# Kernel tuning notes

Measured on AMD Instinct MI355X. Metric: run time of the kernel, lower is better.

## Reference

```python
import jax, jax.numpy as jnp
import numpy as np

IN_CH = 512; OUT_CH = 512; NOISE_SIZE = 512; K = 3; A = 0.2
B = 4; H = 32
_G = float(np.sqrt(2.0 / (1.0 + A * A)))                 # leaky_relu gain, a=0.2
CONV_SCALE = _G / float(np.sqrt(IN_CH * K * K))          # equal-lr kaiming scale (fan_in = in_ch*3*3)
MS_SCALE = float(np.sqrt(2.0 / (NOISE_SIZE + IN_CH)))    # equal-lr xavier scale on make_s linear
RGB_SCALE = _G * float(np.sqrt(2.0 / (OUT_CH + 3)))      # equal-lr xavier scale on 1x1 to_rgb


def upsample2x(x):
    # torch F.interpolate(scale_factor=2, mode='bilinear', align_corners=False)
    b, c, h, w = x.shape
    return jax.image.resize(x, (b, c, 2 * h, 2 * w), method='bilinear')


def mod_conv(x, style, weight, bias, ms_w, ms_b, w_scale, demodulate, pad):
    # style -> per-sample input-channel scales s: (B, Cin)
    s = style @ (ms_w.T * MS_SCALE) + ms_b
    Wmod = (weight * w_scale)[None] * s[:, None, :, None, None]   # (B, Cout, Cin, k, k)
    if demodulate:
        d = jax.lax.rsqrt(jnp.sum(Wmod * Wmod, axis=(2, 3, 4)) + 1e-8)
        Wmod = Wmod * d[:, :, None, None, None]
    conv1 = lambda xi, wi: jax.lax.conv_general_dilated(
        xi[None], wi, (1, 1), [(pad, pad), (pad, pad)],
        dimension_numbers=('NCHW', 'OIHW', 'NCHW'))[0]
    y = jax.vmap(conv1)(x, Wmod)                                   # per-sample weights == grouped conv
    return y + bias[None, :, None, None]


def lrelu(x):
    return jnp.where(x >= 0, x, A * x)


def setup_inputs() -> dict:
    key = jax.random.key(0)
    ks = jax.random.split(key, 19)
    r = lambda i, shape: jax.random.normal(ks[i], shape, dtype=jnp.float32)
    return {
        'maps': r(0, (B, IN_CH, H, H)),
        'w': r(1, (B, NOISE_SIZE)),
        'rgb': r(2, (B, 3, H, H)),
        'noise0': r(3, (B, 1, 2 * H, 2 * H)),
        'noise1': r(4, (B, 1, 2 * H, 2 * H)),
        'conv0_w': r(5, (OUT_CH, IN_CH, K, K)),
        'conv0_b': 0.1 * r(6, (OUT_CH,)),
        'ms0_w': r(7, (IN_CH, NOISE_SIZE)),
        'ms0_b': jnp.ones((IN_CH,), jnp.float32),
        'ns0': 0.1 * r(8, (OUT_CH,)),
        'conv1_w': r(9, (OUT_CH, OUT_CH, K, K)),
        'conv1_b': 0.1 * r(10, (OUT_CH,)),
        'ms1_w': r(11, (OUT_CH, NOISE_SIZE)),
        'ms1_b': jnp.ones((OUT_CH,), jnp.float32),
        'ns1': 0.1 * r(12, (OUT_CH,)),
        'rgb_w': r(13, (3, OUT_CH, 1, 1)),
        'rgb_b': 0.1 * r(14, (3,)),
        'msr_w': r(15, (OUT_CH, NOISE_SIZE)),
        'msr_b': jnp.ones((OUT_CH,), jnp.float32),
    }


def reference(maps, w, rgb, noise0, noise1,
              conv0_w, conv0_b, ms0_w, ms0_b, ns0,
              conv1_w, conv1_b, ms1_w, ms1_b, ns1,
              rgb_w, rgb_b, msr_w, msr_b):
    # upsample branch (upsample=True)
    rgb = upsample2x(rgb)
    maps = upsample2x(maps)
    # layer 0: modulated conv -> noise -> leaky relu
    h = mod_conv(maps, w, conv0_w, conv0_b, ms0_w, ms0_b, CONV_SCALE, True, 1)
    h = lrelu(h + ns0[None, :, None, None] * noise0)
    # layer 1
    h = mod_conv(h, w, conv1_w, conv1_b, ms1_w, ms1_b, CONV_SCALE, True, 1)
    h = lrelu(h + ns1[None, :, None, None] * noise1)
    # to_rgb: 1x1 modulated conv, no demodulation
    rgb_out = rgb + mod_conv(h, w, rgb_w, rgb_b, msr_w, msr_b, RGB_SCALE, False, 0)
    return (rgb_out, h)
```

## Files before the change

### kernel.cpp

```cpp
#include <hip/hip_runtime.h>
#include <stdint.h>


#define BATCH 4
#define CH 512
#define NPP 4356
#define HOUT_OFF 49152

static constexpr double G_GAIN = 1.3867504905630728;
static constexpr float CONV_SCALE_F = (float)(G_GAIN / 67.88225099390857);
static constexpr float MS_SCALE_F = 0.044194173824159216f;
static constexpr float RGB_SCALE_F = (float)(G_GAIN * 1.4142135623730951 / 22.693611435820433);

typedef __attribute__((ext_vector_type(8))) short short8;
typedef __attribute__((ext_vector_type(4))) float floatx4;
typedef __attribute__((ext_vector_type(16))) float floatx16;

#define OFF_S0     256
#define OFF_S1     (OFF_S0 + 8192)
#define OFF_SR     (OFF_S1 + 8192)
#define OFF_D0     (OFF_SR + 8192)
#define OFF_D1     (OFF_D0 + 8192)
#define OFF_B0F    (OFF_D1 + 8192)
#define OFF_B1F    (OFF_B0F + 2048)
#define OFF_NS0F   (OFF_B1F + 2048)
#define OFF_NS1F   (OFF_NS0F + 2048)
#define OFF_WMODR  (OFF_NS1F + 2048)
#define OFF_N0F    (OFF_WMODR + 24576)
#define OFF_N1F    (OFF_N0F + 65536)
#define OFF_WT0    (OFF_N1F + 65536)
#define WT_BYTES   4718592
#define OFF_WT1    (OFF_WT0 + WT_BYTES)
#define OFF_XP0    (OFF_WT1 + WT_BYTES)
#define XP_BYTES   17842176
#define OFF_XP1    (OFF_XP0 + XP_BYTES)

__device__ __forceinline__ float bf2f(unsigned short u) {
  return __uint_as_float(((unsigned int)u) << 16);
}
__device__ __forceinline__ unsigned short f2bf(float f) {
  unsigned int x = __float_as_uint(f);
  unsigned int r = x + 0x7FFFu + ((x >> 16) & 1u);
  return (unsigned short)(r >> 16);
}
__device__ __forceinline__ float ldin(const void* p, long i, int bf) {
  if (bf) return bf2f(((const unsigned short*)p)[i]);
  return ((const float*)p)[i];
}
__device__ __forceinline__ int bfflag_of(const void* msb) {
  return ((const unsigned int*)msb)[0] == 0x3F803F80u ? 1 : 0;
}
__device__ __forceinline__ void async_ld16(const void* g, void* l) {
  __builtin_amdgcn_global_load_lds(
      (const __attribute__((address_space(1))) unsigned int*)g,
      (__attribute__((address_space(3))) unsigned int*)l, 16, 0, 0);
}
__device__ __forceinline__ void upw(int o, int n_in, int& lo, int& hi, float& wlo) {
  int k = o >> 1;
  if (o & 1) { lo = k; hi = k + 1; if (hi > n_in - 1) hi = n_in - 1; wlo = 0.75f; }
  else       { lo = k - 1; if (lo < 0) lo = 0; hi = k; wlo = 0.25f; }
}

__global__ void k_pre(const void* w, const void* msw0, const void* msb0,
                      const void* msw1, const void* msb1,
                      const void* mswr, const void* msbr,
                      const void* b0, const void* b1, const void* nv0,
                      const void* nv1, const void* noise0, const void* noise1,
                      float* s0, float* s1, float* sr,
                      float* ob0, float* ob1, float* ons0, float* ons1,
                      float* on0, float* on1, unsigned short* Xp) {
  const int bf = bfflag_of(msb0);
  const int bid = blockIdx.x;
  if (bid < 264) {
    const int idx = bid * 256 + threadIdx.x;
    const int plane = idx / 132;
    const int rem = idx - plane * 132;
    const int row65 = rem >= 66;
    const int col = rem - (row65 ? 66 : 0);
    const short8 z = {0, 0, 0, 0, 0, 0, 0, 0};
    *(short8*)&Xp[((long)plane * NPP + (row65 ? 65 : 0) * 66 + col) * 8] = z;
    return;
  }
  if (bid < 648) {
    const int b2 = bid - 264;
    const int mat = b2 >> 7, chunk = b2 & 127;
    const int wv = threadIdx.x >> 6, lane = threadIdx.x & 63;
    const int i = chunk * 4 + wv;
    const void* msw; const void* msb; float* out;
    if (mat == 0)      { msw = msw0; msb = msb0; out = s0; }
    else if (mat == 1) { msw = msw1; msb = msb1; out = s1; }
    else               { msw = mswr; msb = msbr; out = sr; }
    float a[4] = {0.f, 0.f, 0.f, 0.f};
    const int n0 = lane * 8;
    if (bf) {
      short8 m8 = *(const short8*)((const unsigned short*)msw + (long)i * 512 + n0);
      for (int b = 0; b < 4; ++b) {
        short8 w8 = *(const short8*)((const unsigned short*)w + b * 512 + n0);
        float s = 0.f;
        for (int e = 0; e < 8; ++e)
          s += bf2f((unsigned short)m8[e]) * bf2f((unsigned short)w8[e]);
        a[b] = s;
      }
    } else {
      const float* mrow = (const float*)msw + (long)i * 512 + n0;
      float4 m0v = *(const float4*)mrow, m1v = *(const float4*)(mrow + 4);
      for (int b = 0; b < 4; ++b) {
        const float* wr = (const float*)w + b * 512 + n0;
        float4 w0v = *(const float4*)wr, w1v = *(const float4*)(wr + 4);
        a[b] = m0v.x * w0v.x + m0v.y * w0v.y + m0v.z * w0v.z + m0v.w * w0v.w +
               m1v.x * w1v.x + m1v.y * w1v.y + m1v.z * w1v.z + m1v.w * w1v.w;
      }
    }
    for (int off = 1; off < 64; off <<= 1)
      for (int b = 0; b < 4; ++b) a[b] += __shfl_xor(a[b], off, 64);
    if (lane == 0) {
      const float mb = ldin(msb, i, bf);
      for (int b = 0; b < 4; ++b) out[b * 512 + i] = a[b] * MS_SCALE_F + mb;
    }
    return;
  }
  const int t = (bid - 648) * 256 + threadIdx.x;
  if (t < 512) {
    ob0[t] = ldin(b0, t, bf); ob1[t] = ldin(b1, t, bf);
    ons0[t] = ldin(nv0, t, bf); ons1[t] = ldin(nv1, t, bf);
  }
  on0[t] = ldin(noise0, t, bf);
  on1[t] = ldin(noise1, t, bf);
}

__global__ void k_mid(const void* w0, const void* w1,
                      const float* s0, const float* s1, const float* sr,
                      const void* rw, unsigned short* Wt0, unsigned short* Wt1,
                      float* S0, float* S1, float* owmr,
                      const void* maps, unsigned short* Xp0, const void* msb) {
  const int bf = bfflag_of(msb);
  const int bid = blockIdx.x;
  __shared__ float smem[32 * 4 * 32];
  if (bid < 256) {
    const int l = bid >> 7, cog = bid & 127;
    const void* w = l ? w1 : w0;
    const float* s = l ? s1 : s0;
    unsigned short* Wt = l ? Wt1 : Wt0;
    float* S = l ? S1 : S0;
    const int co_sub = threadIdx.x >> 6;
    const int kb = (threadIdx.x >> 2) & 15, q = threadIdx.x & 3;
    const int co = cog * 4 + co_sub;
    const int ci0 = kb * 32 + q * 8;
    const long base = ((long)co * 512 + ci0) * 9;
    float v[9][8];
    if (bf) {
      const unsigned short* wp = (const unsigned short*)w + base;
      short8 r[9];
#pragma unroll
      for (int k = 0; k < 9; ++k) r[k] = *(const short8*)(wp + k * 8);
#pragma unroll
      for (int j = 0; j < 8; ++j)
#pragma unroll
        for (int t = 0; t < 9; ++t) {
          const int off = j * 9 + t;
          v[t][j] = bf2f((unsigned short)r[off >> 3][off & 7]);
        }
    } else {
      const float* wp = (const float*)w + base;
      float4 r[18];
#pragma unroll
      for (int k = 0; k < 18; ++k) r[k] = *(const float4*)(wp + k * 4);
#pragma unroll
      for (int j = 0; j < 8; ++j)
#pragma unroll
        for (int t = 0; t < 9; ++t) {
          const int off = j * 9 + t;
          const float4 rr = r[off >> 2];
          const int c2 = off & 3;
          v[t][j] = c2 == 0 ? rr.x : (c2 == 1 ? rr.y : (c2 == 2 ? rr.z : rr.w));
        }
    }
#pragma unroll
    for (int t = 0; t < 9; ++t) {
      short8 pk;
#pragma unroll
      for (int j = 0; j < 8; ++j) pk[j] = (short)f2bf(v[t][j]);
      *(short8*)&Wt[((long)(t * 16 + kb) * 4 + q) * 4096 + co * 8] = pk;
    }
    float wsq[8];
#pragma unroll
    for (int j = 0; j < 8; ++j) {
      float a = 0.f;
#pragma unroll
      for (int t = 0; t < 9; ++t) a += v[t][j] * v[t][j];
      wsq[j] = a;
    }
    float part[4];
#pragma unroll
    for (int b4 = 0; b4 < 4; ++b4) {
      const float* sp = s + b4 * 512 + ci0;
      float4 sa = *(const float4*)sp, sb = *(const float4*)(sp + 4);
      part[b4] = sa.x * sa.x * wsq[0] + sa.y * sa.y * wsq[1] +
                 sa.z * sa.z * wsq[2] + sa.w * sa.w * wsq[3] +
                 sb.x * sb.x * wsq[4] + sb.y * sb.y * wsq[5] +
                 sb.z * sb.z * wsq[6] + sb.w * sb.w * wsq[7];
    }
    for (int off = 1; off < 64; off <<= 1)
#pragma unroll
      for (int b4 = 0; b4 < 4; ++b4)
        part[b4] += __shfl_xor(part[b4], off, 64);
    if ((threadIdx.x & 63) == 0)
#pragma unroll
      for (int b4 = 0; b4 < 4; ++b4) S[b4 * 512 + co] = part[b4];
    return;
  }
  if (bid < 1280) {
    const int bid2 = bid - 256;
    const int t = bid2 & 15, kb = (bid2 >> 4) & 15, b = bid2 >> 8;
    float (*lds)[4][32] = (float(*)[4][32])smem;
    {
      const int ciq = threadIdx.x >> 5;
      const int x = threadIdx.x & 31;
      for (int cc = 0; cc < 4; ++cc) {
        const int ci = cc * 8 + ciq;
        const long cbase = ((long)(b * 512 + kb * 32 + ci)) << 10;
        for (int r = 0; r < 4; ++r) {
          int ir = 2 * t - 1 + r;
          ir = ir < 0 ? 0 : (ir > 31 ? 31 : ir);
          lds[ci][r][x] = ldin(maps, cbase + ir * 32 + x, bf);
        }
      }
    }
    __syncthreads();
    const int q = threadIdx.x >> 6, px = threadIdx.x & 63;
    int xlo, xhi; float wx;
    upw(px, 32, xlo, xhi, wx);
    float sv[8];
    for (int jj = 0; jj < 8; ++jj) sv[jj] = s0[b * 512 + kb * 32 + q * 8 + jj];
    for (int y = 0; y < 4; ++y) {
      const int yg = 4 * t + y;
      int ylo, yhi; float wy;
      upw(yg, 32, ylo, yhi, wy);
      const int rlo = ylo - (2 * t - 1), rhi = yhi - (2 * t - 1);
      short8 pk;
      for (int jj = 0; jj < 8; ++jj) {
        const int ci = q * 8 + jj;
        float vlo = wx * lds[ci][rlo][xlo] + (1.f - wx) * lds[ci][rlo][xhi];
        float vhi = wx * lds[ci][rhi][xlo] + (1.f - wx) * lds[ci][rhi][xhi];
        float v = (wy * vlo + (1.f - wy) * vhi) * sv[jj];
        pk[jj] = (short)f2bf(v);
      }
      *(short8*)&Xp0[((((long)b * 16 + kb) * 4 + q) * NPP + (yg + 1) * 66 + (px + 1)) * 8] = pk;
    }
    return;
  }
  const int i = (bid - 1280) * 256 + threadIdx.x;
  const int b = i / 1536; const int r = i - b * 1536;
  const int c = r >> 9; const int ci = r & 511;
  owmr[i] = RGB_SCALE_F * ldin(rw, c * 512 + ci, bf) * sr[b * 512 + ci];
}

#define MFMA32 __builtin_amdgcn_mfma_f32_32x32x16_bf16
template <int LAYER>
__global__ __launch_bounds__(256, 1) void k_conv(
    const unsigned short* __restrict__ Wt,
    const unsigned short* Xp,
    const float* __restrict__ Ssum,
    const float* __restrict__ bias,
    const float* __restrict__ nsc,
    const float* __restrict__ noise,
    const float* __restrict__ snext,
    unsigned short* XpOut,
    void* dout,
    const void* __restrict__ msb) {
  __shared__ __align__(16) unsigned short AB[49152];
  const int idx = blockIdx.x;
  const int mt = idx & 3, b = (idx >> 2) & 3, nt = idx >> 4;
  const int m0 = mt << 7, y0 = nt << 2;
  const int lane = threadIdx.x & 63, wv = threadIdx.x >> 6;
  const int wm = wv >> 1, wn = wv & 1, wn2 = wn << 1;
  const int l31 = lane & 31, hi = lane >> 5;

  const floatx16 vz = {0.f, 0.f, 0.f, 0.f, 0.f, 0.f, 0.f, 0.f,
                       0.f, 0.f, 0.f, 0.f, 0.f, 0.f, 0.f, 0.f};
  floatx16 d00 = vz, d01 = vz, d02 = vz, d03 = vz;
  floatx16 d10 = vz, d11 = vz, d12 = vz, d13 = vz;

  const int vA32 = (hi << 10) + (wm << 9) + (l31 << 3);
  const int BB = 24576;
  const int vB32   = (hi << 9) + (l31 << 3);
  const int vB32m1 = (hi << 9) + ((l31 == 0 ? 0 : l31 - 1) << 3);
  const int vB32p1 = (hi << 9) + ((l31 == 31 ? 31 : l31 + 1) << 3);
  const bool ee0 = (l31 == 0), ee31 = (l31 == 31);

  auto issueB6 = [&](int kbn, int half) {
#pragma unroll
    for (int k = 0; k < 6; ++k) {
      const int t = wv * 6 + k;
      const int row = t >> 2, qq = t & 3;
      const unsigned short* src =
          Xp + ((((long)b * 16 + kbn) * 4 + qq) * NPP + (long)(y0 + row) * 66 + 1 + lane) * 8;
      async_ld16(src, &AB[BB + half * 12288 + ((row * 4 + qq) << 9)]);
    }
  };
  auto issueA = [&](int kb, int ky, int par) {
#pragma unroll
    for (int k = 0; k < 6; ++k) {
      const int c = wv * 6 + k;
      const int half64 = c & 1, chunk = c >> 1;
      const int kx = chunk >> 2, qq = chunk & 3;
      const unsigned short* src =
          Wt + ((long)(((ky * 3 + kx) * 16 + kb) * 4 + qq) << 12) +
          ((m0 + half64 * 64 + lane) << 3);
      async_ld16(src, &AB[par * 12288 + chunk * 1024 + half64 * 512]);
    }
  };

  const short8 z8 = {0, 0, 0, 0, 0, 0, 0, 0};

#define KSTEP(KX, S)                                                           \
  {                                                                            \
    const int ka = ab + (((KX)*4 + 2*(S)) << 10);                              \
    const int ks = (S) << 10;                                                  \
    short8 a0 = *(const short8*)&AB[ka + vA32];                                \
    short8 a1 = *(const short8*)&AB[ka + vA32 + 256];                          \
    short8 b0, b1, b2, b3;                                                     \
    if ((KX) == 0) {                                                           \
      b0 = *(const short8*)&AB[bo0 + ks + vB32m1];                             \
      b1 = *(const short8*)&AB[bo0 + ks + vB32 + 248];                         \
      b2 = *(const short8*)&AB[bo1 + ks + vB32m1];                             \
      b3 = *(const short8*)&AB[bo1 + ks + vB32 + 248];                         \
      b0 = ee0 ? z8 : b0; b2 = ee0 ? z8 : b2;                                  \
    } else if ((KX) == 1) {                                                    \
      b0 = *(const short8*)&AB[bo0 + ks + vB32];                               \
      b1 = *(const short8*)&AB[bo0 + ks + vB32 + 256];                         \
      b2 = *(const short8*)&AB[bo1 + ks + vB32];                               \
      b3 = *(const short8*)&AB[bo1 + ks + vB32 + 256];                         \
    } else {                                                                   \
      b0 = *(const short8*)&AB[bo0 + ks + vB32 + 8];                           \
      b1 = *(const short8*)&AB[bo0 + ks + vB32p1 + 256];                       \
      b2 = *(const short8*)&AB[bo1 + ks + vB32 + 8];                           \
      b3 = *(const short8*)&AB[bo1 + ks + vB32p1 + 256];                       \
      b1 = ee31 ? z8 : b1; b3 = ee31 ? z8 : b3;                                \
    }                                                                          \
    d00 = MFMA32(a0, b0, d00, 0, 0, 0); d01 = MFMA32(a0, b1, d01, 0, 0, 0);    \
    d02 = MFMA32(a0, b2, d02, 0, 0, 0); d03 = MFMA32(a0, b3, d03, 0, 0, 0);    \
    d10 = MFMA32(a1, b0, d10, 0, 0, 0); d11 = MFMA32(a1, b1, d11, 0, 0, 0);    \
    d12 = MFMA32(a1, b2, d12, 0, 0, 0); d13 = MFMA32(a1, b3, d13, 0, 0, 0);    \
  }

#define RND(KY, PA, HB, KB, NKB, NKY, NPA, DOB, DKB, DHB)                      \
  {                                                                            \
    __syncthreads();                                                           \
    issueA((NKB), (NKY), (NPA));                                               \
    if (DOB) issueB6((DKB), (DHB));                                            \
    const int ab = (PA) * 12288;                                               \
    const int bo0 = BB + (HB) * 12288 + ((wn2 + (KY)) << 11);                  \
    const int bo1 = bo0 + 2048;                                                \
    KSTEP(0, 0) KSTEP(0, 1)                                                    \
    KSTEP(1, 0) KSTEP(1, 1)                                                    \
    KSTEP(2, 0) KSTEP(2, 1)                                                    \
  }

  issueA(0, 0, 0);
  issueB6(0, 0);

#pragma unroll 1
  for (int it = 0; it < 8; ++it) {
    const int kb = it * 2, kb1 = kb + 1, kb2 = (kb + 2) & 15;
    RND(0, 0, 0, kb,  kb,  1, 1, 1, kb1, 1)
    RND(1, 1, 0, kb,  kb,  2, 0, 0, 0,  0)
    RND(2, 0, 0, kb,  kb1, 0, 1, 0, 0,  0)
    RND(0, 1, 1, kb1, kb1, 1, 0, 1, kb2, 0)
    RND(1, 0, 1, kb1, kb1, 2, 1, 0, 0,  0)
    RND(2, 1, 1, kb1, kb2, 0, 0, 0, 0,  0)
  }
#undef RND
#undef KSTEP

  floatx16 accv[2][4] = {{d00, d01, d02, d03}, {d10, d11, d12, d13}};
  const int bfflag = bfflag_of(msb);
  const int cb = m0 + (wm << 6);
#pragma unroll
  for (int i = 0; i < 2; ++i) {
#pragma unroll
    for (int g = 0; g < 4; ++g) {
      const int cg = cb + i * 32 + g * 8 + 4 * hi;
      float Ds[4], bi[4], nv[4], sx[4];
#pragma unroll
      for (int r = 0; r < 4; ++r) {
        float Sv = Ssum[b * 512 + cg + r];
        Ds[r] = CONV_SCALE_F * rsqrtf(CONV_SCALE_F * CONV_SCALE_F * Sv + 1e-8f);
        bi[r] = bias[cg + r];
        nv[r] = nsc[cg + r];
        sx[r] = (LAYER == 0) ? snext[b * 512 + cg + r] : 0.f;
      }
#pragma unroll
      for (int j = 0; j < 4; ++j) {
        const int y = y0 + wn2 + (j >> 1);
        const int x = ((j & 1) << 5) + l31;
        const int p = (y << 6) + x;
        const float nz = noise[b * 4096 + p];
        if (LAYER == 0) {
          unsigned long long pk = 0ull;
#pragma unroll
          for (int r = 0; r < 4; ++r) {
            float v = accv[i][j][g * 4 + r] * Ds[r] + bi[r] + nv[r] * nz;
            v = (v >= 0.f) ? v : 0.2f * v;
            pk |= (unsigned long long)f2bf(v * sx[r]) << (16 * r);
          }
          const int pp = (y + 1) * 66 + (x + 1);
          const long o = ((((long)b * 16 + (cg >> 5)) * 4 + ((cg >> 3) & 3)) * NPP + pp) * 8 + (cg & 7);
          *(unsigned long long*)(XpOut + o) = pk;
        } else {
#pragma unroll
          for (int r = 0; r < 4; ++r) {
            float v = accv[i][j][g * 4 + r] * Ds[r] + bi[r] + nv[r] * nz;
            v = (v >= 0.f) ? v : 0.2f * v;
            const long o = (((long)(b * 512 + cg + r)) << 12) + p;
            if (bfflag) ((unsigned short*)dout)[HOUT_OFF + o] = f2bf(v);
            else        ((float*)dout)[HOUT_OFF + o] = v;
          }
        }
      }
    }
  }
}

__global__ void k_rgb(const void* rgb_in, const float* wmodr, const void* rb,
                      void* dout, const void* msb) {
  const int bf = bfflag_of(msb);
  const int b = blockIdx.y, p0 = blockIdx.x * 512;
  const int g = threadIdx.x >> 6, lane = threadIdx.x & 63;
  const int px = p0 + lane * 8;
  const char* hbytes = (const char*)dout + (long)HOUT_OFF * (bf ? 2 : 4);
  const float* wm = wmodr + b * 1536;
  float a0[8] = {}, a1[8] = {}, a2[8] = {};
  for (int ci = g * 128; ci < g * 128 + 128; ++ci) {
    const long o = (((long)(b * 512 + ci)) << 12) + px;
    float hv[8];
    if (bf) {
      short8 h8 = *(const short8*)((const unsigned short*)hbytes + o);
#pragma unroll
      for (int k = 0; k < 8; ++k) hv[k] = bf2f((unsigned short)h8[k]);
    } else {
      float4 f0 = *(const float4*)((const float*)hbytes + o);
      float4 f1 = *(const float4*)((const float*)hbytes + o + 4);
      hv[0] = f0.x; hv[1] = f0.y; hv[2] = f0.z; hv[3] = f0.w;
      hv[4] = f1.x; hv[5] = f1.y; hv[6] = f1.z; hv[7] = f1.w;
    }
    const float w0 = wm[ci], w1 = wm[512 + ci], w2 = wm[1024 + ci];
#pragma unroll
    for (int k = 0; k < 8; ++k) {
      a0[k] += w0 * hv[k]; a1[k] += w1 * hv[k]; a2[k] += w2 * hv[k];
    }
  }
  __shared__ float red[4][3][512];
#pragma unroll
  for (int k = 0; k < 8; ++k) {
    red[g][0][lane * 8 + k] = a0[k];
    red[g][1][lane * 8 + k] = a1[k];
    red[g][2][lane * 8 + k] = a2[k];
  }
  __syncthreads();
  for (int e = 0; e < 2; ++e) {
    const int pp = threadIdx.x * 2 + e;
    const int p = p0 + pp;
    const int y = p >> 6, x = p & 63;
    int ylo, yhi, xlo, xhi; float wy, wx;
    upw(y, 32, ylo, yhi, wy);
    upw(x, 32, xlo, xhi, wx);
    for (int c = 0; c < 3; ++c) {
      float s = red[0][c][pp] + red[1][c][pp] + red[2][c][pp] + red[3][c][pp];
      const long base = (long)(b * 3 + c) << 10;
      const float v00 = ldin(rgb_in, base + ylo * 32 + xlo, bf);
      const float v01 = ldin(rgb_in, base + ylo * 32 + xhi, bf);
      const float v10 = ldin(rgb_in, base + yhi * 32 + xlo, bf);
      const float v11 = ldin(rgb_in, base + yhi * 32 + xhi, bf);
      const float up = wy * (wx * v00 + (1.f - wx) * v01) +
                       (1.f - wy) * (wx * v10 + (1.f - wx) * v11);
      const float v = up + s + ldin(rb, c, bf);
      const long o = ((long)(b * 3 + c) << 12) + p;
      if (bf) ((unsigned short*)dout)[o] = f2bf(v);
      else    ((float*)dout)[o] = v;
    }
  }
}

extern "C" void kernel_launch(void* const* d_in, const int* in_sizes, int n_in,
                              void* d_out, int out_size, void* d_ws, size_t ws_size,
                              hipStream_t stream) {
  char* ws = (char*)d_ws;
  float* s0 = (float*)(ws + OFF_S0);
  float* s1 = (float*)(ws + OFF_S1);
  float* sr = (float*)(ws + OFF_SR);
  float* S0 = (float*)(ws + OFF_D0);
  float* S1 = (float*)(ws + OFF_D1);
  float* b0f = (float*)(ws + OFF_B0F);
  float* b1f = (float*)(ws + OFF_B1F);
  float* ns0f = (float*)(ws + OFF_NS0F);
  float* ns1f = (float*)(ws + OFF_NS1F);
  float* wmodr = (float*)(ws + OFF_WMODR);
  float* n0f = (float*)(ws + OFF_N0F);
  float* n1f = (float*)(ws + OFF_N1F);
  unsigned short* Wt0 = (unsigned short*)(ws + OFF_WT0);
  unsigned short* Wt1 = (unsigned short*)(ws + OFF_WT1);
  unsigned short* Xp0 = (unsigned short*)(ws + OFF_XP0);
  unsigned short* Xp1 = (unsigned short*)(ws + OFF_XP1);

  k_pre<<<712, 256, 0, stream>>>(d_in[1], d_in[7], d_in[8], d_in[12], d_in[13],
                                 d_in[17], d_in[18], d_in[6], d_in[11], d_in[9],
                                 d_in[14], d_in[3], d_in[4],
                                 s0, s1, sr, b0f, b1f, ns0f, ns1f, n0f, n1f, Xp0);
  k_mid<<<1304, 256, 0, stream>>>(d_in[5], d_in[10], s0, s1, sr, d_in[15],
                                  Wt0, Wt1, S0, S1, wmodr, d_in[0], Xp0, d_in[8]);
  k_conv<0><<<256, 256, 0, stream>>>(Wt0, Xp0, S0, b0f, ns0f, n0f, s1, Xp1,
                                     d_out, d_in[8]);
  k_conv<1><<<256, 256, 0, stream>>>(Wt1, Xp1, S1, b1f, ns1f, n1f, s1, Xp1,
                                     d_out, d_in[8]);
  k_rgb<<<dim3(8, 4), 256, 0, stream>>>(d_in[2], wmodr, d_in[16], d_out, d_in[8]);
  (void)in_sizes; (void)n_in; (void)out_size; (void)ws_size;
}
```

Measured before the change: 306.4 us.

## Split conv K-reduction across two wave groups with LDS accumulator reduction

```diff
diff --git a/kernel.cpp b/kernel.cpp
--- a/kernel.cpp
+++ b/kernel.cpp
@@ -257,7 +257,7 @@
 
 #define MFMA32 __builtin_amdgcn_mfma_f32_32x32x16_bf16
 template <int LAYER>
-__global__ __launch_bounds__(256, 1) void k_conv(
+__global__ __launch_bounds__(512, 2) void k_conv(
     const unsigned short* __restrict__ Wt,
     const unsigned short* Xp,
     const float* __restrict__ Ssum,
@@ -273,7 +273,7 @@
   const int mt = idx & 3, b = (idx >> 2) & 3, nt = idx >> 4;
   const int m0 = mt << 7, y0 = nt << 2;
   const int lane = threadIdx.x & 63, wv = threadIdx.x >> 6;
-  const int wm = wv >> 1, wn = wv & 1, wn2 = wn << 1;
+  const int kh = wv >> 2, wm = (wv >> 1) & 1, wp = wv & 1, wp2 = wp << 1;
   const int l31 = lane & 31, hi = lane >> 5;
 
   const floatx16 vz = {0.f, 0.f, 0.f, 0.f, 0.f, 0.f, 0.f, 0.f,
@@ -281,17 +281,17 @@
   floatx16 d00 = vz, d01 = vz, d02 = vz, d03 = vz;
   floatx16 d10 = vz, d11 = vz, d12 = vz, d13 = vz;
 
-  const int vA32 = (hi << 10) + (wm << 9) + (l31 << 3);
+  const int vA32k = (kh << 11) + (hi << 10) + (wm << 9) + (l31 << 3);
   const int BB = 24576;
-  const int vB32   = (hi << 9) + (l31 << 3);
-  const int vB32m1 = (hi << 9) + ((l31 == 0 ? 0 : l31 - 1) << 3);
-  const int vB32p1 = (hi << 9) + ((l31 == 31 ? 31 : l31 + 1) << 3);
+  const int vB32k   = (kh << 10) + (hi << 9) + (l31 << 3);
+  const int vB32km1 = (kh << 10) + (hi << 9) + ((l31 == 0 ? 0 : l31 - 1) << 3);
+  const int vB32kp1 = (kh << 10) + (hi << 9) + ((l31 == 31 ? 31 : l31 + 1) << 3);
   const bool ee0 = (l31 == 0), ee31 = (l31 == 31);
 
   auto issueB6 = [&](int kbn, int half) {
 #pragma unroll
-    for (int k = 0; k < 6; ++k) {
-      const int t = wv * 6 + k;
+    for (int k = 0; k < 3; ++k) {
+      const int t = wv * 3 + k;
       const int row = t >> 2, qq = t & 3;
       const unsigned short* src =
           Xp + ((((long)b * 16 + kbn) * 4 + qq) * NPP + (long)(y0 + row) * 66 + 1 + lane) * 8;
@@ -300,8 +300,8 @@
   };
   auto issueA = [&](int kb, int ky, int par) {
 #pragma unroll
-    for (int k = 0; k < 6; ++k) {
-      const int c = wv * 6 + k;
+    for (int k = 0; k < 3; ++k) {
+      const int c = wv * 3 + k;
       const int half64 = c & 1, chunk = c >> 1;
       const int kx = chunk >> 2, qq = chunk & 3;
       const unsigned short* src =
@@ -313,29 +313,28 @@
 
   const short8 z8 = {0, 0, 0, 0, 0, 0, 0, 0};
 
-#define KSTEP(KX, S)                                                           \
+#define KSTEP(KX)                                                              \
   {                                                                            \
-    const int ka = ab + (((KX)*4 + 2*(S)) << 10);                              \
-    const int ks = (S) << 10;                                                  \
-    short8 a0 = *(const short8*)&AB[ka + vA32];                                \
-    short8 a1 = *(const short8*)&AB[ka + vA32 + 256];                          \
+    const int ka = ab + ((KX) << 12);                                          \
+    short8 a0 = *(const short8*)&AB[ka + vA32k];                               \
+    short8 a1 = *(const short8*)&AB[ka + vA32k + 256];                         \
     short8 b0, b1, b2, b3;                                                     \
     if ((KX) == 0) {                                                           \
-      b0 = *(const short8*)&AB[bo0 + ks + vB32m1];                             \
-      b1 = *(const short8*)&AB[bo0 + ks + vB32 + 248];                         \
-      b2 = *(const short8*)&AB[bo1 + ks + vB32m1];                             \
-      b3 = *(const short8*)&AB[bo1 + ks + vB32 + 248];                         \
+      b0 = *(const short8*)&AB[bo0 + vB32km1];                                 \
+      b1 = *(const short8*)&AB[bo0 + vB32k + 248];                             \
+      b2 = *(const short8*)&AB[bo1 + vB32km1];                                 \
+      b3 = *(const short8*)&AB[bo1 + vB32k + 248];                             \
       b0 = ee0 ? z8 : b0; b2 = ee0 ? z8 : b2;                                  \
     } else if ((KX) == 1) {                                                    \
-      b0 = *(const short8*)&AB[bo0 + ks + vB32];                               \
-      b1 = *(const short8*)&AB[bo0 + ks + vB32 + 256];                         \
-      b2 = *(const short8*)&AB[bo1 + ks + vB32];                               \
-      b3 = *(const short8*)&AB[bo1 + ks + vB32 + 256];                         \
+      b0 = *(const short8*)&AB[bo0 + vB32k];                                   \
+      b1 = *(const short8*)&AB[bo0 + vB32k + 256];                             \
+      b2 = *(const short8*)&AB[bo1 + vB32k];                                   \
+      b3 = *(const short8*)&AB[bo1 + vB32k + 256];                             \
     } else {                                                                   \
-      b0 = *(const short8*)&AB[bo0 + ks + vB32 + 8];                           \
-      b1 = *(const short8*)&AB[bo0 + ks + vB32p1 + 256];                       \
-      b2 = *(const short8*)&AB[bo1 + ks + vB32 + 8];                           \
-      b3 = *(const short8*)&AB[bo1 + ks + vB32p1 + 256];                       \
+      b0 = *(const short8*)&AB[bo0 + vB32k + 8];                               \
+      b1 = *(const short8*)&AB[bo0 + vB32kp1 + 256];                           \
+      b2 = *(const short8*)&AB[bo1 + vB32k + 8];                               \
+      b3 = *(const short8*)&AB[bo1 + vB32kp1 + 256];                           \
       b1 = ee31 ? z8 : b1; b3 = ee31 ? z8 : b3;                                \
     }                                                                          \
     d00 = MFMA32(a0, b0, d00, 0, 0, 0); d01 = MFMA32(a0, b1, d01, 0, 0, 0);    \
@@ -350,11 +349,9 @@
     issueA((NKB), (NKY), (NPA));                                               \
     if (DOB) issueB6((DKB), (DHB));                                            \
     const int ab = (PA) * 12288;                                               \
-    const int bo0 = BB + (HB) * 12288 + ((wn2 + (KY)) << 11);                  \
+    const int bo0 = BB + (HB) * 12288 + ((wp2 + (KY)) << 11);                  \
     const int bo1 = bo0 + 2048;                                                \
-    KSTEP(0, 0) KSTEP(0, 1)                                                    \
-    KSTEP(1, 0) KSTEP(1, 1)                                                    \
-    KSTEP(2, 0) KSTEP(2, 1)                                                    \
+    KSTEP(0) KSTEP(1) KSTEP(2)                                                 \
   }
 
   issueA(0, 0, 0);
@@ -373,48 +370,76 @@
 #undef RND
 #undef KSTEP
 
-  floatx16 accv[2][4] = {{d00, d01, d02, d03}, {d10, d11, d12, d13}};
-  const int bfflag = bfflag_of(msb);
-  const int cb = m0 + (wm << 6);
-#pragma unroll
-  for (int i = 0; i < 2; ++i) {
-#pragma unroll
-    for (int g = 0; g < 4; ++g) {
-      const int cg = cb + i * 32 + g * 8 + 4 * hi;
-      float Ds[4], bi[4], nv[4], sx[4];
-#pragma unroll
-      for (int r = 0; r < 4; ++r) {
-        float Sv = Ssum[b * 512 + cg + r];
-        Ds[r] = CONV_SCALE_F * rsqrtf(CONV_SCALE_F * CONV_SCALE_F * Sv + 1e-8f);
-        bi[r] = bias[cg + r];
-        nv[r] = nsc[cg + r];
-        sx[r] = (LAYER == 0) ? snext[b * 512 + cg + r] : 0.f;
-      }
-#pragma unroll
-      for (int j = 0; j < 4; ++j) {
-        const int y = y0 + wn2 + (j >> 1);
-        const int x = ((j & 1) << 5) + l31;
-        const int p = (y << 6) + x;
-        const float nz = noise[b * 4096 + p];
-        if (LAYER == 0) {
-          unsigned long long pk = 0ull;
-#pragma unroll
-          for (int r = 0; r < 4; ++r) {
-            float v = accv[i][j][g * 4 + r] * Ds[r] + bi[r] + nv[r] * nz;
-            v = (v >= 0.f) ? v : 0.2f * v;
-            pk |= (unsigned long long)f2bf(v * sx[r]) << (16 * r);
-          }
-          const int pp = (y + 1) * 66 + (x + 1);
-          const long o = ((((long)b * 16 + (cg >> 5)) * 4 + ((cg >> 3) & 3)) * NPP + pp) * 8 + (cg & 7);
-          *(unsigned long long*)(XpOut + o) = pk;
-        } else {
-#pragma unroll
-          for (int r = 0; r < 4; ++r) {
-            float v = accv[i][j][g * 4 + r] * Ds[r] + bi[r] + nv[r] * nz;
-            v = (v >= 0.f) ? v : 0.2f * v;
-            const long o = (((long)(b * 512 + cg + r)) << 12) + p;
-            if (bfflag) ((unsigned short*)dout)[HOUT_OFF + o] = f2bf(v);
-            else        ((float*)dout)[HOUT_OFF + o] = v;
+  {
+    float* Rf = (float*)AB;
+    const int wq = wv & 3;
+#define STACC(V, T)                                                            \
+    { _Pragma("unroll") for (int s = 0; s < 4; ++s) {                          \
+        floatx4 t4 = {V[4*s+0], V[4*s+1], V[4*s+2], V[4*s+3]};                 \
+        *(floatx4*)&Rf[((wq * 16 + (T) * 4 + s) << 8) + (lane << 2)] = t4;     \
+      } }
+#define LDACC(V, T)                                                            \
+    { _Pragma("unroll") for (int s = 0; s < 4; ++s) {                          \
+        floatx4 t4 = *(const floatx4*)&Rf[((wq * 16 + (T) * 4 + s) << 8) + (lane << 2)]; \
+        V[4*s+0] += t4[0]; V[4*s+1] += t4[1];                                  \
+        V[4*s+2] += t4[2]; V[4*s+3] += t4[3];                                  \
+      } }
+    __syncthreads();
+    if (kh) { STACC(d00, 0) STACC(d01, 1) STACC(d02, 2) STACC(d03, 3) }
+    __syncthreads();
+    if (!kh) { LDACC(d00, 0) LDACC(d01, 1) LDACC(d02, 2) LDACC(d03, 3) }
+    __syncthreads();
+    if (kh) { STACC(d10, 0) STACC(d11, 1) STACC(d12, 2) STACC(d13, 3) }
+    __syncthreads();
+    if (!kh) { LDACC(d10, 0) LDACC(d11, 1) LDACC(d12, 2) LDACC(d13, 3) }
+#undef STACC
+#undef LDACC
+  }
+
+  if (kh == 0) {
+    floatx16 accv[2][4] = {{d00, d01, d02, d03}, {d10, d11, d12, d13}};
+    const int bfflag = bfflag_of(msb);
+    const int cb = m0 + (wm << 6);
+#pragma unroll
+    for (int i = 0; i < 2; ++i) {
+#pragma unroll
+      for (int g = 0; g < 4; ++g) {
+        const int cg = cb + i * 32 + g * 8 + 4 * hi;
+        float Ds[4], bi[4], nv[4], sx[4];
+#pragma unroll
+        for (int r = 0; r < 4; ++r) {
+          float Sv = Ssum[b * 512 + cg + r];
+          Ds[r] = CONV_SCALE_F * rsqrtf(CONV_SCALE_F * CONV_SCALE_F * Sv + 1e-8f);
+          bi[r] = bias[cg + r];
+          nv[r] = nsc[cg + r];
+          sx[r] = (LAYER == 0) ? snext[b * 512 + cg + r] : 0.f;
+        }
+#pragma unroll
+        for (int j = 0; j < 4; ++j) {
+          const int y = y0 + wp2 + (j >> 1);
+          const int x = ((j & 1) << 5) + l31;
+          const int p = (y << 6) + x;
+          const float nz = noise[b * 4096 + p];
+          if (LAYER == 0) {
+            unsigned long long pk = 0ull;
+#pragma unroll
+            for (int r = 0; r < 4; ++r) {
+              float v = accv[i][j][g * 4 + r] * Ds[r] + bi[r] + nv[r] * nz;
+              v = (v >= 0.f) ? v : 0.2f * v;
+              pk |= (unsigned long long)f2bf(v * sx[r]) << (16 * r);
+            }
+            const int pp = (y + 1) * 66 + (x + 1);
+            const long o = ((((long)b * 16 + (cg >> 5)) * 4 + ((cg >> 3) & 3)) * NPP + pp) * 8 + (cg & 7);
+            *(unsigned long long*)(XpOut + o) = pk;
+          } else {
+#pragma unroll
+            for (int r = 0; r < 4; ++r) {
+              float v = accv[i][j][g * 4 + r] * Ds[r] + bi[r] + nv[r] * nz;
+              v = (v >= 0.f) ? v : 0.2f * v;
+              const long o = (((long)(b * 512 + cg + r)) << 12) + p;
+              if (bfflag) ((unsigned short*)dout)[HOUT_OFF + o] = f2bf(v);
+              else        ((float*)dout)[HOUT_OFF + o] = v;
+            }
           }
         }
       }
@@ -509,9 +534,9 @@
                                  s0, s1, sr, b0f, b1f, ns0f, ns1f, n0f, n1f, Xp0);
   k_mid<<<1304, 256, 0, stream>>>(d_in[5], d_in[10], s0, s1, sr, d_in[15],
                                   Wt0, Wt1, S0, S1, wmodr, d_in[0], Xp0, d_in[8]);
-  k_conv<0><<<256, 256, 0, stream>>>(Wt0, Xp0, S0, b0f, ns0f, n0f, s1, Xp1,
+  k_conv<0><<<256, 512, 0, stream>>>(Wt0, Xp0, S0, b0f, ns0f, n0f, s1, Xp1,
                                      d_out, d_in[8]);
-  k_conv<1><<<256, 256, 0, stream>>>(Wt1, Xp1, S1, b1f, ns1f, n1f, s1, Xp1,
+  k_conv<1><<<256, 512, 0, stream>>>(Wt1, Xp1, S1, b1f, ns1f, n1f, s1, Xp1,
                                      d_out, d_in[8]);
   k_rgb<<<dim3(8, 4), 256, 0, stream>>>(d_in[2], wmodr, d_in[16], d_out, d_in[8]);
   (void)in_sizes; (void)n_in; (void)out_size; (void)ws_size;
```

Measured after the change: 315.9 us. +3.1%, slower.
